# Kernel optimization log

Measured on AMD Instinct MI355X. Metric: run time of the kernel, lower is better.

The kernel has to match this reference:

```python
import jax, jax.numpy as jnp
import numpy as np

N = 50000   # nodes
E = 800000  # edges (before self loops)
NEG_SLOPE = 0.2
EPS_BN = 1e-5
EPS_SM = 1e-16  # PyG softmax denominator epsilon


def gat_conv(x, src, dst, W, att_src, att_dst, bias, heads, ch):
    n = x.shape[0]
    xh = (x @ W).reshape(n, heads, ch)                       # [N,H,C]
    a_src = jnp.sum(xh * att_src, axis=-1)                   # [N,H]
    a_dst = jnp.sum(xh * att_dst, axis=-1)                   # [N,H]
    e = a_src[src] + a_dst[dst]                              # [E,H]
    e = jax.nn.leaky_relu(e, NEG_SLOPE)
    m = jax.ops.segment_max(e, dst, num_segments=n)          # segment softmax
    ex = jnp.exp(e - m[dst])
    denom = jax.ops.segment_sum(ex, dst, num_segments=n)
    alpha = ex / (denom[dst] + EPS_SM)                       # [E,H]
    msg = alpha[:, :, None] * xh[src]                        # [E,H,C]
    out = jax.ops.segment_sum(msg, dst, num_segments=n)      # [N,H,C]
    return out.reshape(n, heads * ch) + bias


def batch_norm(x, gamma, beta):
    mu = jnp.mean(x, axis=0)
    var = jnp.mean((x - mu) ** 2, axis=0)
    return (x - mu) * jax.lax.rsqrt(var + EPS_BN) * gamma + beta


def setup_inputs() -> dict:
    key = jax.random.key(0)
    ks = jax.random.split(key, 16)
    d = {}
    d['x'] = jax.random.normal(ks[0], (N, 128), jnp.float32)
    d['edge_index'] = jax.random.randint(ks[1], (2, E), 0, N, dtype=jnp.int64)
    d['W1'] = jax.random.normal(ks[2], (128, 256), jnp.float32) * 0.1
    d['as1'] = jax.random.normal(ks[3], (2, 128), jnp.float32) * 0.1
    d['ad1'] = jax.random.normal(ks[4], (2, 128), jnp.float32) * 0.1
    d['b1'] = jax.random.normal(ks[5], (256,), jnp.float32) * 0.1
    d['g1'] = jnp.ones((256,), jnp.float32)
    d['be1'] = jnp.zeros((256,), jnp.float32)
    d['W2'] = jax.random.normal(ks[6], (256, 128), jnp.float32) * 0.1
    d['as2'] = jax.random.normal(ks[7], (2, 64), jnp.float32) * 0.1
    d['ad2'] = jax.random.normal(ks[8], (2, 64), jnp.float32) * 0.1
    d['b2'] = jax.random.normal(ks[9], (128,), jnp.float32) * 0.1
    d['g2'] = jnp.ones((128,), jnp.float32)
    d['be2'] = jnp.zeros((128,), jnp.float32)
    d['W3'] = jax.random.normal(ks[10], (128, 128), jnp.float32) * 0.1
    d['as3'] = jax.random.normal(ks[11], (2, 64), jnp.float32) * 0.1
    d['ad3'] = jax.random.normal(ks[12], (2, 64), jnp.float32) * 0.1
    d['b3'] = jax.random.normal(ks[13], (128,), jnp.float32) * 0.1
    d['lw'] = jax.random.normal(ks[14], (128, 64), jnp.float32) * 0.1
    d['lb'] = jnp.zeros((64,), jnp.float32)
    return d


def reference(x, edge_index, W1, as1, ad1, b1, g1, be1,
              W2, as2, ad2, b2, g2, be2,
              W3, as3, ad3, b3, lw, lb):
    # add self loops (PyG GATConv default add_self_loops=True)
    loops = jnp.arange(N, dtype=edge_index.dtype)
    src = jnp.concatenate([edge_index[0], loops])
    dst = jnp.concatenate([edge_index[1], loops])

    h = jax.nn.relu(gat_conv(x, src, dst, W1, as1, ad1, b1, 2, 128))   # [N,256]
    h = batch_norm(h, g1, be1)
    h = jax.nn.relu(gat_conv(h, src, dst, W2, as2, ad2, b2, 2, 64))    # [N,128]
    h = batch_norm(h, g2, be2)
    h = jax.nn.relu(gat_conv(h, src, dst, W3, as3, ad3, b3, 2, 64))    # [N,128]
    return h @ lw + lb                                                 # [N,64]
```

## Files before the change

### kernel.cpp

```cpp
#include <hip/hip_runtime.h>
#include <hip/hip_bf16.h>

#define NEG_SLOPE 0.2f
#define EPS_BN 1e-5f
#define EPS_SM 1e-16f
#define CAP 128

typedef __bf16 bf16x8 __attribute__((ext_vector_type(8)));
typedef __bf16 bf16x4 __attribute__((ext_vector_type(4)));
typedef float floatx4 __attribute__((ext_vector_type(4)));

__device__ __forceinline__ float leaky(float x) { return x > 0.f ? x : NEG_SLOPE * x; }

__global__ void k_detect(const int* __restrict__ ei, int* __restrict__ cnt, int e) {
    int i = threadIdx.x + blockIdx.x * blockDim.x;
    if (i < 1024 && 2 * i + 1 < 2 * e) {
        if (ei[2 * i + 1] != 0) atomicAdd(cnt, 1);
    }
}

__global__ void k_hist_wconv(const int* __restrict__ ei, const int* __restrict__ cnt,
                             int* __restrict__ deg, int* __restrict__ col, int e, int ebase,
                             const float* __restrict__ W1, __bf16* __restrict__ Wb1,
                             const float* __restrict__ W2, __bf16* __restrict__ Wb2,
                             const float* __restrict__ W3, __bf16* __restrict__ Wb3) {
    int g = threadIdx.x + blockIdx.x * blockDim.x;
    if (g < e) {
        bool is64 = (*cnt) < 512;
        int s = is64 ? ei[2 * g] : ei[g];
        int d = is64 ? ei[2 * (e + g)] : ei[e + g];
        int r = atomicAdd(&deg[d], 1);
        if (r < CAP) col[((size_t)d << 7) + r] = s;
    } else {
        int idx = g - ebase;
        if (idx >= 0 && idx < 32768) {
            int mm = idx >> 7, kk = idx & 127;
            Wb1[idx] = (__bf16)W1[(size_t)kk * 256 + mm];
        } else if (idx < 65536) {
            int i2 = idx - 32768;
            int mm = i2 >> 8, kk = i2 & 255;
            Wb2[i2] = (__bf16)W2[(size_t)kk * 128 + mm];
        } else if (idx < 81920) {
            int i3 = idx - 65536;
            int mm = i3 >> 7, kk = i3 & 127;
            Wb3[i3] = (__bf16)W3[(size_t)kk * 128 + mm];
        }
    }
}

template <int K, int LC, bool BF16IN, int NT>
__global__ __launch_bounds__(256) void k_gemm(const void* __restrict__ Ain,
                                              const __bf16* __restrict__ Bt,
                                              __bf16* __restrict__ Cb, int n, int M,
                                              const float* __restrict__ bnsums,
                                              const float* __restrict__ gam,
                                              const float* __restrict__ bet,
                                              const float* __restrict__ att_s,
                                              const float* __restrict__ att_d,
                                              float* __restrict__ asrc,
                                              float* __restrict__ adst) {
    __shared__ __align__(16) __bf16 As[128][72];
    __shared__ __align__(16) __bf16 Bs[NT * 16][72];
    __shared__ float sc_lds[K], sh_lds[K];
    const int row0 = blockIdx.y * 128, col0 = blockIdx.x * (NT * 16);
    const int lane = threadIdx.x & 63, w = threadIdx.x >> 6;
    const int m = lane & 15, quad = lane >> 4;

    if (bnsums) {
        for (int c = threadIdx.x; c < K; c += 256) {
            float mean = bnsums[c] / n;
            float var = bnsums[256 + c] / n - mean * mean;
            float sc = gam[c] * rsqrtf(var + EPS_BN);
            sc_lds[c] = sc;
            sh_lds[c] = bet[c] - mean * sc;
        }
        __syncthreads();
    }

    floatx4 acc[2][NT];
#pragma unroll
    for (int i = 0; i < 2; ++i)
#pragma unroll
        for (int j = 0; j < NT; ++j) acc[i][j] = (floatx4)0.f;

    const int sr = threadIdx.x >> 1;
    const int sk = (threadIdx.x & 1) * 32;

    for (int kc = 0; kc < K; kc += 64) {
        {
            int grow = row0 + sr;
            if (grow < n) {
                if (BF16IN) {
                    const __bf16* p = (const __bf16*)Ain + (size_t)grow * K + kc + sk;
#pragma unroll
                    for (int q = 0; q < 4; ++q) {
                        bf16x8 vv = *reinterpret_cast<const bf16x8*>(p + q * 8);
                        if (bnsums) {
                            int c = kc + sk + q * 8;
                            bf16x8 r;
#pragma unroll
                            for (int e2 = 0; e2 < 8; ++e2)
                                r[e2] = (__bf16)((float)vv[e2] * sc_lds[c + e2] + sh_lds[c + e2]);
                            vv = r;
                        }
                        *reinterpret_cast<bf16x8*>(&As[sr][sk + q * 8]) = vv;
                    }
                } else {
                    const float* p = (const float*)Ain + (size_t)grow * K + kc + sk;
#pragma unroll
                    for (int q = 0; q < 8; ++q) {
                        float4 v = *reinterpret_cast<const float4*>(p + q * 4);
                        bf16x4 cv = {(__bf16)v.x, (__bf16)v.y, (__bf16)v.z, (__bf16)v.w};
                        *reinterpret_cast<bf16x4*>(&As[sr][sk + q * 4]) = cv;
                    }
                }
            } else {
#pragma unroll
                for (int q = 0; q < 4; ++q)
                    *reinterpret_cast<bf16x8*>(&As[sr][sk + q * 8]) = (bf16x8)(__bf16)0.f;
            }
        }
        if (NT == 8) {
            const __bf16* p = Bt + (size_t)(col0 + sr) * K + kc + sk;
#pragma unroll
            for (int q = 0; q < 4; ++q)
                *reinterpret_cast<bf16x8*>(&Bs[sr][sk + q * 8]) =
                    *reinterpret_cast<const bf16x8*>(p + q * 8);
        } else {
            int sr4 = threadIdx.x >> 2, sk4 = (threadIdx.x & 3) * 16;
            const __bf16* p = Bt + (size_t)(col0 + sr4) * K + kc + sk4;
            *reinterpret_cast<bf16x8*>(&Bs[sr4][sk4]) = *reinterpret_cast<const bf16x8*>(p);
            *reinterpret_cast<bf16x8*>(&Bs[sr4][sk4 + 8]) = *reinterpret_cast<const bf16x8*>(p + 8);
        }
        __syncthreads();
#pragma unroll
        for (int ks = 0; ks < 64; ks += 32) {
            bf16x8 a0 = *reinterpret_cast<const bf16x8*>(&As[w * 32 + m][ks + quad * 8]);
            bf16x8 a1 = *reinterpret_cast<const bf16x8*>(&As[w * 32 + 16 + m][ks + quad * 8]);
#pragma unroll
            for (int nt = 0; nt < NT; ++nt) {
                bf16x8 b = *reinterpret_cast<const bf16x8*>(&Bs[nt * 16 + m][ks + quad * 8]);
                acc[0][nt] = __builtin_amdgcn_mfma_f32_16x16x32_bf16(a0, b, acc[0][nt], 0, 0, 0);
                acc[1][nt] = __builtin_amdgcn_mfma_f32_16x16x32_bf16(a1, b, acc[1][nt], 0, 0, 0);
            }
        }
        __syncthreads();
    }
#pragma unroll
    for (int mt = 0; mt < 2; ++mt)
#pragma unroll
        for (int nt = 0; nt < NT; ++nt)
#pragma unroll
            for (int r = 0; r < 4; ++r) {
                int row = row0 + w * 32 + mt * 16 + quad * 4 + r;
                if (row < n) Cb[(size_t)row * M + col0 + nt * 16 + m] = (__bf16)acc[mt][nt][r];
            }
    {
        float asv[NT], adv[NT];
#pragma unroll
        for (int nt = 0; nt < NT; ++nt) {
            int c = col0 + nt * 16 + m;
            asv[nt] = att_s[c];
            adv[nt] = att_d[c];
        }
        const int h = (col0 >> LC) & 1;
#pragma unroll
        for (int mt = 0; mt < 2; ++mt)
#pragma unroll
            for (int r = 0; r < 4; ++r) {
                int row = row0 + w * 32 + mt * 16 + quad * 4 + r;
                float pa = 0.f, pb = 0.f;
#pragma unroll
                for (int nt = 0; nt < NT; ++nt) {
                    float v = acc[mt][nt][r];
                    pa += v * asv[nt];
                    pb += v * adv[nt];
                }
#pragma unroll
                for (int off = 1; off <= 8; off <<= 1) {
                    pa += __shfl_xor(pa, off);
                    pb += __shfl_xor(pb, off);
                }
                if (m == 0 && row < n) {
                    atomicAdd(asrc + 2 * row + h, pa);
                    atomicAdd(adst + 2 * row + h, pb);
                }
            }
    }
}

__global__ __launch_bounds__(256) void k_lin(const float* __restrict__ A,
                                             const float* __restrict__ lw,
                                             const float* __restrict__ lb,
                                             float* __restrict__ out, int n) {
    __shared__ __align__(16) __bf16 Ahi[64][136];
    __shared__ __align__(16) __bf16 Alo[64][136];
    __shared__ __align__(16) __bf16 Bhi[64][136];
    const int row0 = blockIdx.x * 64;
    const int lane = threadIdx.x & 63, w = threadIdx.x >> 6;
    const int m = lane & 15, quad = lane >> 4;
    floatx4 acc[4];
#pragma unroll
    for (int i = 0; i < 4; ++i) acc[i] = (floatx4)0.f;
    {
        int sr = threadIdx.x >> 2, sk0 = (threadIdx.x & 3) * 32;
        int grow = row0 + sr;
#pragma unroll
        for (int q = 0; q < 8; ++q) {
            float4 v = make_float4(0.f, 0.f, 0.f, 0.f);
            if (grow < n) v = *reinterpret_cast<const float4*>(A + (size_t)grow * 128 + sk0 + q * 4);
            float vv[4] = {v.x, v.y, v.z, v.w};
#pragma unroll
            for (int i = 0; i < 4; ++i) {
                __bf16 h = (__bf16)vv[i];
                Ahi[sr][sk0 + q * 4 + i] = h;
                Alo[sr][sk0 + q * 4 + i] = (__bf16)(vv[i] - (float)h);
            }
        }
    }
    {
        int k0 = threadIdx.x >> 1, m0 = (threadIdx.x & 1) * 32;
#pragma unroll
        for (int q = 0; q < 8; ++q) {
            float4 v = *reinterpret_cast<const float4*>(lw + (size_t)k0 * 64 + m0 + q * 4);
            float vv[4] = {v.x, v.y, v.z, v.w};
#pragma unroll
            for (int i = 0; i < 4; ++i) Bhi[m0 + q * 4 + i][k0] = (__bf16)vv[i];
        }
    }
    __syncthreads();
#pragma unroll
    for (int ks = 0; ks < 128; ks += 32) {
        bf16x8 ah = *reinterpret_cast<const bf16x8*>(&Ahi[w * 16 + m][ks + quad * 8]);
        bf16x8 al = *reinterpret_cast<const bf16x8*>(&Alo[w * 16 + m][ks + quad * 8]);
#pragma unroll
        for (int nt = 0; nt < 4; ++nt) {
            bf16x8 bh = *reinterpret_cast<const bf16x8*>(&Bhi[nt * 16 + m][ks + quad * 8]);
            acc[nt] = __builtin_amdgcn_mfma_f32_16x16x32_bf16(ah, bh, acc[nt], 0, 0, 0);
            acc[nt] = __builtin_amdgcn_mfma_f32_16x16x32_bf16(al, bh, acc[nt], 0, 0, 0);
        }
    }
#pragma unroll
    for (int nt = 0; nt < 4; ++nt)
#pragma unroll
        for (int r = 0; r < 4; ++r) {
            int row = row0 + w * 16 + quad * 4 + r;
            int c = nt * 16 + m;
            if (row < n) out[(size_t)row * 64 + c] = acc[nt][r] + lb[c];
        }
}

template <int C, bool OUTBF16>
__global__ __launch_bounds__(256) void k_agg(const __bf16* __restrict__ xh,
                                             const float* __restrict__ asrc,
                                             const float* __restrict__ adst,
                                             const int* __restrict__ degv,
                                             const int* __restrict__ col,
                                             const float* __restrict__ bias,
                                             void* __restrict__ outv, int n) {
    constexpr int F = 2 * C;
    constexpr int G = F / 8;
    constexpr int NG = 64 / G;
    constexpr int GSH = (G == 32) ? 5 : 4;
    __shared__ float4 slots[4][80];
    const int widx = threadIdx.x >> 6;
    const int node = blockIdx.x * 4 + widx;
    const int lane = threadIdx.x & 63;
    if (node >= n) return;
    const int t = lane & (G - 1);
    const int g = lane >> GSH;
    const bool h1 = (t * 8) >= C;
    if (lane >= 48) slots[widx][lane + 16] = make_float4(0.f, 0.f, 0.f, 0.f);
    const int* crow = col + ((size_t)node << 7);
    const int deg = min(degv[node], CAP);
    const float2 adv = *reinterpret_cast<const float2*>(adst + 2 * node);
    const float2 asv = *reinterpret_cast<const float2*>(asrc + 2 * node);
    const float es0 = leaky(asv.x + adv.x), es1 = leaky(asv.y + adv.y);
    float acc[8] = {};
    float d0 = 0.f, d1 = 0.f;
    for (int base = 0; base < deg; base += 64) {
        const int cnt = min(64, deg - base);
        float4 sv = make_float4(0.f, 0.f, 0.f, 0.f);
        if (lane < cnt) {
            int s = crow[base + lane];
            float2 av = *reinterpret_cast<const float2*>(asrc + 2 * s);
            float w0 = __expf(leaky(av.x + adv.x));
            float w1 = __expf(leaky(av.y + adv.y));
            d0 += w0; d1 += w1;
            sv = make_float4(__int_as_float(s * (F * 2)), w0, w1, 0.f);
        }
        slots[widx][lane] = sv;
        for (int j = g; j < cnt; j += 4 * NG) {
            float4 s0 = slots[widx][j];
            float4 s1 = slots[widx][j + NG];
            float4 s2 = slots[widx][j + 2 * NG];
            float4 s3 = slots[widx][j + 3 * NG];
            const char* xb = (const char*)xh;
            bf16x8 v0 = *reinterpret_cast<const bf16x8*>(xb + (unsigned)__float_as_int(s0.x) + t * 16);
            bf16x8 v1 = *reinterpret_cast<const bf16x8*>(xb + (unsigned)__float_as_int(s1.x) + t * 16);
            bf16x8 v2 = *reinterpret_cast<const bf16x8*>(xb + (unsigned)__float_as_int(s2.x) + t * 16);
            bf16x8 v3 = *reinterpret_cast<const bf16x8*>(xb + (unsigned)__float_as_int(s3.x) + t * 16);
            float w0 = h1 ? s0.z : s0.y;
            float w1 = h1 ? s1.z : s1.y;
            float w2 = h1 ? s2.z : s2.y;
            float w3 = h1 ? s3.z : s3.y;
#pragma unroll
            for (int q = 0; q < 8; ++q)
                acc[q] += w0 * (float)v0[q] + w1 * (float)v1[q] +
                          w2 * (float)v2[q] + w3 * (float)v3[q];
        }
    }
#pragma unroll
    for (int off = 1; off <= 32; off <<= 1) {
        d0 += __shfl_xor(d0, off);
        d1 += __shfl_xor(d1, off);
    }
#pragma unroll
    for (int q = 0; q < 8; ++q) {
#pragma unroll
        for (int off = G; off < 64; off <<= 1) acc[q] += __shfl_xor(acc[q], off);
    }
    float exs0 = __expf(es0), exs1 = __expf(es1);
    d0 += exs0; d1 += exs1;
    {
        float ws = h1 ? exs1 : exs0;
        bf16x8 v = *reinterpret_cast<const bf16x8*>(xh + (size_t)node * F + t * 8);
#pragma unroll
        for (int q = 0; q < 8; ++q) acc[q] += ws * (float)v[q];
    }
    float inv = 1.0f / ((h1 ? d1 : d0) + EPS_SM);
    float o[8];
#pragma unroll
    for (int q = 0; q < 8; ++q) o[q] = fmaxf(acc[q] * inv + bias[t * 8 + q], 0.f);
    if (g == 0) {
        if constexpr (OUTBF16) {
            __bf16* po = (__bf16*)outv + (size_t)node * F + t * 8;
            bf16x8 st;
#pragma unroll
            for (int q = 0; q < 8; ++q) st[q] = (__bf16)o[q];
            *reinterpret_cast<bf16x8*>(po) = st;
        } else {
            float* po = (float*)outv + (size_t)node * F + t * 8;
            *reinterpret_cast<float4*>(po) = make_float4(o[0], o[1], o[2], o[3]);
            *reinterpret_cast<float4*>(po + 4) = make_float4(o[4], o[5], o[6], o[7]);
        }
    }
}

template <typename T>
__global__ void k_bn_stats(const T* __restrict__ x, float* __restrict__ sums,
                           float* __restrict__ sqs, int n, int f) {
    int c = threadIdx.x;
    float s = 0.f, q = 0.f;
    for (int r = blockIdx.x; r < n; r += gridDim.x) {
        float v = (float)x[(size_t)r * f + c];
        s += v; q += v * v;
    }
    atomicAdd(&sums[c], s);
    atomicAdd(&sqs[c], q);
}

extern "C" void kernel_launch(void* const* d_in, const int* in_sizes, int n_in,
                              void* d_out, int out_size, void* d_ws, size_t ws_size,
                              hipStream_t stream) {
    const float* x   = (const float*)d_in[0];
    const int*   ei  = (const int*)d_in[1];
    const float* W1  = (const float*)d_in[2];
    const float* as1 = (const float*)d_in[3];
    const float* ad1 = (const float*)d_in[4];
    const float* b1  = (const float*)d_in[5];
    const float* g1  = (const float*)d_in[6];
    const float* be1 = (const float*)d_in[7];
    const float* W2  = (const float*)d_in[8];
    const float* as2 = (const float*)d_in[9];
    const float* ad2 = (const float*)d_in[10];
    const float* b2  = (const float*)d_in[11];
    const float* g2  = (const float*)d_in[12];
    const float* be2 = (const float*)d_in[13];
    const float* W3  = (const float*)d_in[14];
    const float* as3 = (const float*)d_in[15];
    const float* ad3 = (const float*)d_in[16];
    const float* b3  = (const float*)d_in[17];
    const float* lw  = (const float*)d_in[18];
    const float* lb  = (const float*)d_in[19];
    float* outp = (float*)d_out;

    const int n = in_sizes[0] / 128;
    const int e = in_sizes[1] / 2;

    char* w = (char*)d_ws;
    size_t off = 0;
    auto alloc = [&](size_t bytes) -> void* {
        void* p = w + off;
        off += (bytes + 255) & ~(size_t)255;
        return p;
    };
    __bf16* xhb = (__bf16*)alloc((size_t)n * 256 * 2);
    __bf16* h1b = (__bf16*)alloc((size_t)n * 256 * 2);
    __bf16* h2b = (__bf16*)alloc((size_t)n * 128 * 2);
    float*  h3f = (float*)alloc((size_t)n * 128 * 4);
    int* colb   = (int*)alloc((size_t)n * CAP * 4);
    __bf16* Wb1 = (__bf16*)alloc(256 * 128 * 2);
    __bf16* Wb2 = (__bf16*)alloc(128 * 256 * 2);
    __bf16* Wb3 = (__bf16*)alloc(128 * 128 * 2);
    char* zb_begin = (char*)(w + off);
    int* deg    = (int*)alloc((size_t)n * 4);
    float* bn1  = (float*)alloc(512 * 4);
    float* bn2  = (float*)alloc(512 * 4);
    int* dcnt   = (int*)alloc(256);
    float* as1p = (float*)alloc((size_t)n * 2 * 4);
    float* ad1p = (float*)alloc((size_t)n * 2 * 4);
    float* as2p = (float*)alloc((size_t)n * 2 * 4);
    float* ad2p = (float*)alloc((size_t)n * 2 * 4);
    float* as3p = (float*)alloc((size_t)n * 2 * 4);
    float* ad3p = (float*)alloc((size_t)n * 2 * 4);
    char* zb_end = (char*)(w + off);

    hipMemsetAsync(zb_begin, 0, (size_t)(zb_end - zb_begin), stream);

    k_detect<<<4, 256, 0, stream>>>(ei, dcnt, e);
    const int ebase = ((e + 255) / 256) * 256;
    const int histblocks = ebase / 256 + 320;
    k_hist_wconv<<<histblocks, 256, 0, stream>>>(ei, dcnt, deg, colb, e, ebase,
                                                 W1, Wb1, W2, Wb2, W3, Wb3);

    const int nwb = (n + 3) / 4;
    const int nrow = (n + 127) / 128;

    k_gemm<128, 7, false, 8><<<dim3(2, nrow), 256, 0, stream>>>(
        x, Wb1, xhb, n, 256, nullptr, nullptr, nullptr, as1, ad1, as1p, ad1p);
    k_agg<128, true><<<nwb, 256, 0, stream>>>(xhb, as1p, ad1p, deg, colb, b1, h1b, n);
    k_bn_stats<__bf16><<<256, 256, 0, stream>>>(h1b, bn1, bn1 + 256, n, 256);

    k_gemm<256, 6, true, 4><<<dim3(2, nrow), 256, 0, stream>>>(
        h1b, Wb2, xhb, n, 128, bn1, g1, be1, as2, ad2, as2p, ad2p);
    k_agg<64, true><<<nwb, 256, 0, stream>>>(xhb, as2p, ad2p, deg, colb, b2, h2b, n);
    k_bn_stats<__bf16><<<256, 128, 0, stream>>>(h2b, bn2, bn2 + 256, n, 128);

    k_gemm<128, 6, true, 4><<<dim3(2, nrow), 256, 0, stream>>>(
        h2b, Wb3, xhb, n, 128, bn2, g2, be2, as3, ad3, as3p, ad3p);
    k_agg<64, false><<<nwb, 256, 0, stream>>>(xhb, as3p, ad3p, deg, colb, b3, h3f, n);

    k_lin<<<(n + 63) / 64, 256, 0, stream>>>(h3f, lw, lb, outp, n);
}
```

Before: 466.3 us.

## Fuse final linear into last aggregation, merge init kernels, drop atomics

Removes the separate final linear kernel by having the last aggregation kernel stage the transposed linear weight in shared memory and compute each node's 64 outputs directly. The fp32 h3 intermediate and its round trip through global memory go away. The memset and detect kernels are merged into one init kernel that zeroes the degree and BN buffers and decides the index width with a block reduction. The attention-score atomics in the GEMM are replaced with plain stores, which is valid only if each row and head is written exactly once. In exchange, every aggregation block now loads a 32 KB weight tile, the final projection runs as scalar fp32 FMAs rather than MFMA, and the hbuf read has no barrier or wave-level sync after the lane-0 group writes it.

New measurement: 489.0 us. 1.05x slower.

```diff
diff --git a/kernel.cpp b/kernel.cpp
--- a/kernel.cpp
+++ b/kernel.cpp
@@ -12,21 +12,34 @@
 
 __device__ __forceinline__ float leaky(float x) { return x > 0.f ? x : NEG_SLOPE * x; }
 
-__global__ void k_detect(const int* __restrict__ ei, int* __restrict__ cnt, int e) {
-    int i = threadIdx.x + blockIdx.x * blockDim.x;
-    if (i < 1024 && 2 * i + 1 < 2 * e) {
-        if (ei[2 * i + 1] != 0) atomicAdd(cnt, 1);
-    }
-}
-
-__global__ void k_hist_wconv(const int* __restrict__ ei, const int* __restrict__ cnt,
+__global__ void k_init(const int* __restrict__ ei, int* __restrict__ flag,
+                       int* __restrict__ zbase, int zwords, int e) {
+    if (blockIdx.x == 0) {
+        __shared__ int cnt_s[256];
+        int i = threadIdx.x;
+        int nz = (2 * i + 1 < 2 * e && ei[2 * i + 1] != 0) ? 1 : 0;
+        cnt_s[i] = nz;
+        __syncthreads();
+        for (int off = 128; off > 0; off >>= 1) {
+            if (i < off) cnt_s[i] += cnt_s[i + off];
+            __syncthreads();
+        }
+        if (i == 0) *flag = (cnt_s[0] < 128) ? 1 : 0;
+        return;
+    }
+    int g = (blockIdx.x - 1) * 256 + threadIdx.x;
+    int stride = (gridDim.x - 1) * 256;
+    for (int k = g; k < zwords; k += stride) zbase[k] = 0;
+}
+
+__global__ void k_hist_wconv(const int* __restrict__ ei, const int* __restrict__ flag,
                              int* __restrict__ deg, int* __restrict__ col, int e, int ebase,
                              const float* __restrict__ W1, __bf16* __restrict__ Wb1,
                              const float* __restrict__ W2, __bf16* __restrict__ Wb2,
                              const float* __restrict__ W3, __bf16* __restrict__ Wb3) {
     int g = threadIdx.x + blockIdx.x * blockDim.x;
     if (g < e) {
-        bool is64 = (*cnt) < 512;
+        bool is64 = (*flag) != 0;
         int s = is64 ? ei[2 * g] : ei[g];
         int d = is64 ? ei[2 * (e + g)] : ei[e + g];
         int r = atomicAdd(&deg[d], 1);
@@ -182,90 +195,40 @@
                     pb += __shfl_xor(pb, off);
                 }
                 if (m == 0 && row < n) {
-                    atomicAdd(asrc + 2 * row + h, pa);
-                    atomicAdd(adst + 2 * row + h, pb);
+                    asrc[2 * row + h] = pa;
+                    adst[2 * row + h] = pb;
                 }
             }
     }
 }
 
-__global__ __launch_bounds__(256) void k_lin(const float* __restrict__ A,
-                                             const float* __restrict__ lw,
-                                             const float* __restrict__ lb,
-                                             float* __restrict__ out, int n) {
-    __shared__ __align__(16) __bf16 Ahi[64][136];
-    __shared__ __align__(16) __bf16 Alo[64][136];
-    __shared__ __align__(16) __bf16 Bhi[64][136];
-    const int row0 = blockIdx.x * 64;
-    const int lane = threadIdx.x & 63, w = threadIdx.x >> 6;
-    const int m = lane & 15, quad = lane >> 4;
-    floatx4 acc[4];
-#pragma unroll
-    for (int i = 0; i < 4; ++i) acc[i] = (floatx4)0.f;
-    {
-        int sr = threadIdx.x >> 2, sk0 = (threadIdx.x & 3) * 32;
-        int grow = row0 + sr;
-#pragma unroll
-        for (int q = 0; q < 8; ++q) {
-            float4 v = make_float4(0.f, 0.f, 0.f, 0.f);
-            if (grow < n) v = *reinterpret_cast<const float4*>(A + (size_t)grow * 128 + sk0 + q * 4);
-            float vv[4] = {v.x, v.y, v.z, v.w};
-#pragma unroll
-            for (int i = 0; i < 4; ++i) {
-                __bf16 h = (__bf16)vv[i];
-                Ahi[sr][sk0 + q * 4 + i] = h;
-                Alo[sr][sk0 + q * 4 + i] = (__bf16)(vv[i] - (float)h);
-            }
-        }
-    }
-    {
-        int k0 = threadIdx.x >> 1, m0 = (threadIdx.x & 1) * 32;
-#pragma unroll
-        for (int q = 0; q < 8; ++q) {
-            float4 v = *reinterpret_cast<const float4*>(lw + (size_t)k0 * 64 + m0 + q * 4);
-            float vv[4] = {v.x, v.y, v.z, v.w};
-#pragma unroll
-            for (int i = 0; i < 4; ++i) Bhi[m0 + q * 4 + i][k0] = (__bf16)vv[i];
-        }
-    }
-    __syncthreads();
-#pragma unroll
-    for (int ks = 0; ks < 128; ks += 32) {
-        bf16x8 ah = *reinterpret_cast<const bf16x8*>(&Ahi[w * 16 + m][ks + quad * 8]);
-        bf16x8 al = *reinterpret_cast<const bf16x8*>(&Alo[w * 16 + m][ks + quad * 8]);
-#pragma unroll
-        for (int nt = 0; nt < 4; ++nt) {
-            bf16x8 bh = *reinterpret_cast<const bf16x8*>(&Bhi[nt * 16 + m][ks + quad * 8]);
-            acc[nt] = __builtin_amdgcn_mfma_f32_16x16x32_bf16(ah, bh, acc[nt], 0, 0, 0);
-            acc[nt] = __builtin_amdgcn_mfma_f32_16x16x32_bf16(al, bh, acc[nt], 0, 0, 0);
-        }
-    }
-#pragma unroll
-    for (int nt = 0; nt < 4; ++nt)
-#pragma unroll
-        for (int r = 0; r < 4; ++r) {
-            int row = row0 + w * 16 + quad * 4 + r;
-            int c = nt * 16 + m;
-            if (row < n) out[(size_t)row * 64 + c] = acc[nt][r] + lb[c];
-        }
-}
-
-template <int C, bool OUTBF16>
+template <int C, bool OUTBF16, bool FINAL>
 __global__ __launch_bounds__(256) void k_agg(const __bf16* __restrict__ xh,
                                              const float* __restrict__ asrc,
                                              const float* __restrict__ adst,
                                              const int* __restrict__ degv,
                                              const int* __restrict__ col,
                                              const float* __restrict__ bias,
-                                             void* __restrict__ outv, int n) {
+                                             void* __restrict__ outv, int n,
+                                             const float* __restrict__ lw,
+                                             const float* __restrict__ lb) {
     constexpr int F = 2 * C;
     constexpr int G = F / 8;
     constexpr int NG = 64 / G;
     constexpr int GSH = (G == 32) ? 5 : 4;
     __shared__ float4 slots[4][80];
+    __shared__ float lwt[FINAL ? 64 : 1][FINAL ? 129 : 1];
+    __shared__ float hbuf[FINAL ? 4 : 1][FINAL ? 128 : 1];
     const int widx = threadIdx.x >> 6;
     const int node = blockIdx.x * 4 + widx;
     const int lane = threadIdx.x & 63;
+    if constexpr (FINAL) {
+        for (int idx = threadIdx.x; idx < 8192; idx += 256) {
+            int k = idx >> 6, mm = idx & 63;
+            lwt[mm][k] = lw[(size_t)k * 64 + mm];
+        }
+        __syncthreads();
+    }
     if (node >= n) return;
     const int t = lane & (G - 1);
     const int g = lane >> GSH;
@@ -332,7 +295,16 @@
     float o[8];
 #pragma unroll
     for (int q = 0; q < 8; ++q) o[q] = fmaxf(acc[q] * inv + bias[t * 8 + q], 0.f);
-    if (g == 0) {
+    if constexpr (FINAL) {
+        if (g == 0) {
+#pragma unroll
+            for (int q = 0; q < 8; ++q) hbuf[widx][t * 8 + q] = o[q];
+        }
+        float accl = lb[lane];
+#pragma unroll 8
+        for (int c = 0; c < 128; ++c) accl += hbuf[widx][c] * lwt[lane][c];
+        ((float*)outv)[(size_t)node * 64 + lane] = accl;
+    } else if (g == 0) {
         if constexpr (OUTBF16) {
             __bf16* po = (__bf16*)outv + (size_t)node * F + t * 8;
             bf16x8 st;
@@ -398,30 +370,29 @@
     __bf16* xhb = (__bf16*)alloc((size_t)n * 256 * 2);
     __bf16* h1b = (__bf16*)alloc((size_t)n * 256 * 2);
     __bf16* h2b = (__bf16*)alloc((size_t)n * 128 * 2);
-    float*  h3f = (float*)alloc((size_t)n * 128 * 4);
     int* colb   = (int*)alloc((size_t)n * CAP * 4);
     __bf16* Wb1 = (__bf16*)alloc(256 * 128 * 2);
     __bf16* Wb2 = (__bf16*)alloc(128 * 256 * 2);
     __bf16* Wb3 = (__bf16*)alloc(128 * 128 * 2);
-    char* zb_begin = (char*)(w + off);
-    int* deg    = (int*)alloc((size_t)n * 4);
-    float* bn1  = (float*)alloc(512 * 4);
-    float* bn2  = (float*)alloc(512 * 4);
-    int* dcnt   = (int*)alloc(256);
+    int* flag   = (int*)alloc(256);
     float* as1p = (float*)alloc((size_t)n * 2 * 4);
     float* ad1p = (float*)alloc((size_t)n * 2 * 4);
     float* as2p = (float*)alloc((size_t)n * 2 * 4);
     float* ad2p = (float*)alloc((size_t)n * 2 * 4);
     float* as3p = (float*)alloc((size_t)n * 2 * 4);
     float* ad3p = (float*)alloc((size_t)n * 2 * 4);
+    char* zb_begin = (char*)(w + off);
+    int* deg    = (int*)alloc((size_t)n * 4);
+    float* bn1  = (float*)alloc(512 * 4);
+    float* bn2  = (float*)alloc(512 * 4);
     char* zb_end = (char*)(w + off);
-
-    hipMemsetAsync(zb_begin, 0, (size_t)(zb_end - zb_begin), stream);
-
-    k_detect<<<4, 256, 0, stream>>>(ei, dcnt, e);
+    const int zwords = (int)((zb_end - zb_begin) / 4);
+
+    k_init<<<65, 256, 0, stream>>>(ei, flag, (int*)zb_begin, zwords, e);
+
     const int ebase = ((e + 255) / 256) * 256;
     const int histblocks = ebase / 256 + 320;
-    k_hist_wconv<<<histblocks, 256, 0, stream>>>(ei, dcnt, deg, colb, e, ebase,
+    k_hist_wconv<<<histblocks, 256, 0, stream>>>(ei, flag, deg, colb, e, ebase,
                                                  W1, Wb1, W2, Wb2, W3, Wb3);
 
     const int nwb = (n + 3) / 4;
@@ -429,17 +400,18 @@
 
     k_gemm<128, 7, false, 8><<<dim3(2, nrow), 256, 0, stream>>>(
         x, Wb1, xhb, n, 256, nullptr, nullptr, nullptr, as1, ad1, as1p, ad1p);
-    k_agg<128, true><<<nwb, 256, 0, stream>>>(xhb, as1p, ad1p, deg, colb, b1, h1b, n);
+    k_agg<128, true, false><<<nwb, 256, 0, stream>>>(
+        xhb, as1p, ad1p, deg, colb, b1, h1b, n, nullptr, nullptr);
     k_bn_stats<__bf16><<<256, 256, 0, stream>>>(h1b, bn1, bn1 + 256, n, 256);
 
     k_gemm<256, 6, true, 4><<<dim3(2, nrow), 256, 0, stream>>>(
         h1b, Wb2, xhb, n, 128, bn1, g1, be1, as2, ad2, as2p, ad2p);
-    k_agg<64, true><<<nwb, 256, 0, stream>>>(xhb, as2p, ad2p, deg, colb, b2, h2b, n);
+    k_agg<64, true, false><<<nwb, 256, 0, stream>>>(
+        xhb, as2p, ad2p, deg, colb, b2, h2b, n, nullptr, nullptr);
     k_bn_stats<__bf16><<<256, 128, 0, stream>>>(h2b, bn2, bn2 + 256, n, 128);
 
     k_gemm<128, 6, true, 4><<<dim3(2, nrow), 256, 0, stream>>>(
         h2b, Wb3, xhb, n, 128, bn2, g2, be2, as3, ad3, as3p, ad3p);
-    k_agg<64, false><<<nwb, 256, 0, stream>>>(xhb, as3p, ad3p, deg, colb, b3, h3f, n);
-
-    k_lin<<<(n + 63) / 64, 256, 0, stream>>>(h3f, lw, lb, outp, n);
-}
+    k_agg<64, false, true><<<nwb, 256, 0, stream>>>(
+        xhb, as3p, ad3p, deg, colb, b3, outp, n, lw, lb);
+}
```
